# Kernel tuning notes

Hardware: AMD Instinct MI355X
Metric: run time of the kernel (lower is better)

Reference implementation:

```python
import jax, jax.numpy as jnp
import numpy as np

HIDDEN = 2048
HEADS = 16
HEAD_DIM = HIDDEN // HEADS
TOP_K = 256
B, N = 1, 2048


def setup_inputs() -> dict:
    key = jax.random.key(0)
    ks = jax.random.split(key, 9)
    s = 0.02
    return {
        "hidden_states": jax.random.normal(ks[0], (B, N, HIDDEN), jnp.float32),
        "Wq": jax.random.normal(ks[1], (HIDDEN, HIDDEN), jnp.float32) * s,
        "bq": jnp.zeros((HIDDEN,), jnp.float32),
        "Wk": jax.random.normal(ks[2], (HIDDEN, HIDDEN), jnp.float32) * s,
        "bk": jnp.zeros((HIDDEN,), jnp.float32),
        "Wv": jax.random.normal(ks[3], (HIDDEN, HIDDEN), jnp.float32) * s,
        "bv": jnp.zeros((HIDDEN,), jnp.float32),
        "Wo": jax.random.normal(ks[4], (HIDDEN, HIDDEN), jnp.float32) * s,
        "bo": jnp.zeros((HIDDEN,), jnp.float32),
    }


def _split_heads(x):
    b, n, _ = x.shape
    return x.reshape(b, n, HEADS, HEAD_DIM).transpose(0, 2, 1, 3)  # b h n d


def reference(hidden_states, Wq, bq, Wk, bk, Wv, bv, Wo, bo):
    scale = 1.0 / jnp.sqrt(jnp.float32(HEAD_DIM))
    q = _split_heads(hidden_states @ Wq + bq)  # [b,h,n,d]
    k = _split_heads(hidden_states @ Wk + bk)
    v = _split_heads(hidden_states @ Wv + bv)

    # Sparse path (kv_seq_length > attention_window): dense QK^T used only to rank keys.
    scores = jnp.einsum("bhnd,bhmd->bhnm", q, k) * scale  # [b,h,n,n]
    importance = scores.mean(axis=2)  # [b,h,n] aggregate over queries
    _, idx = jax.lax.top_k(importance, TOP_K)  # [b,h,k]

    # gather selected K/V (torch.gather along seq dim)
    k_sel = jnp.take_along_axis(k, idx[..., None], axis=2)  # [b,h,k,d]
    v_sel = jnp.take_along_axis(v, idx[..., None], axis=2)

    w = jax.nn.softmax(jnp.einsum("bhnd,bhkd->bhnk", q, k_sel) * scale, axis=-1)
    out = jnp.einsum("bhnk,bhkd->bhnd", w, v_sel)  # [b,h,n,d]
    out = out.transpose(0, 2, 1, 3).reshape(hidden_states.shape[0], -1, HIDDEN)
    return out @ Wo + bo
```

## Files before the change

### kernel.cpp

```cpp
#include <hip/hip_runtime.h>


typedef __attribute__((ext_vector_type(8))) short bf16x8;
typedef __attribute__((ext_vector_type(4))) float f32x4;

__device__ __forceinline__ unsigned short f2bf(float x) {
    unsigned u = __float_as_uint(x);
    u += 0x7fffu + ((u >> 16) & 1u);
    return (unsigned short)(u >> 16);
}

__device__ __forceinline__ void load_lds16(const unsigned short* g, unsigned short* l) {
    __builtin_amdgcn_global_load_lds(
        (const __attribute__((address_space(1))) unsigned int*)g,
        (__attribute__((address_space(3))) unsigned int*)l,
        16, 0, 0);
}

struct Bias3 { const float* p0; const float* p1; const float* p2; };
struct Ptr4  { const float* p[4]; };

template <int TN, bool OUT_BF16>
__global__ __launch_bounds__(256) void gemm_bf16(
    const unsigned short* __restrict__ A, long lda, long strideA,
    const unsigned short* __restrict__ Bt, long ldb, long strideB,
    void* __restrict__ Cv, long ldc, long strideC,
    Bias3 bias, int K, float alpha)
{
    constexpr int SN = TN / 32;
    __shared__ __align__(16) unsigned short As[128][32];
    __shared__ __align__(16) unsigned short Bs[TN][32];

    const int tid  = threadIdx.x;
    const int lane = tid & 63;
    const int wave = tid >> 6;
    const int wm = wave >> 1, wn = wave & 1;

    const int bm = blockIdx.y * 128;
    const int bn = blockIdx.x * TN;
    const int b  = blockIdx.z;

    const unsigned short* Ab = A  + (long)b * strideA;
    const unsigned short* Bb = Bt + (long)b * strideB;

    f32x4 acc[4][SN];
#pragma unroll
    for (int i = 0; i < 4; i++)
#pragma unroll
        for (int j = 0; j < SN; j++) acc[i][j] = f32x4{0.f, 0.f, 0.f, 0.f};

    const int lr = lane >> 2;
    const int lc = (lane & 3) * 8;

    for (int k0 = 0; k0 < K; k0 += 32) {
        __syncthreads();
#pragma unroll
        for (int r0 = wave * 16; r0 < 128; r0 += 64)
            load_lds16(Ab + (long)(bm + r0 + lr) * lda + k0 + lc, &As[r0][0]);
#pragma unroll
        for (int r0 = wave * 16; r0 < TN; r0 += 64)
            load_lds16(Bb + (long)(bn + r0 + lr) * ldb + k0 + lc, &Bs[r0][0]);
        __syncthreads();

        bf16x8 af[4], bf[SN];
#pragma unroll
        for (int s = 0; s < 4; s++)
            af[s] = *(const bf16x8*)&As[wm * 64 + s * 16 + (lane & 15)][(lane >> 4) * 8];
#pragma unroll
        for (int t = 0; t < SN; t++)
            bf[t] = *(const bf16x8*)&Bs[wn * (TN / 2) + t * 16 + (lane & 15)][(lane >> 4) * 8];
#pragma unroll
        for (int s = 0; s < 4; s++)
#pragma unroll
            for (int t = 0; t < SN; t++)
                acc[s][t] = __builtin_amdgcn_mfma_f32_16x16x32_bf16(af[s], bf[t], acc[s][t], 0, 0, 0);
    }

    const float* bp = (b == 0) ? bias.p0 : (b == 1) ? bias.p1 : bias.p2;
    float* Cf = (float*)Cv;
    unsigned short* Ch = (unsigned short*)Cv;
#pragma unroll
    for (int s = 0; s < 4; s++) {
#pragma unroll
        for (int t = 0; t < SN; t++) {
            const int col  = bn + wn * (TN / 2) + t * 16 + (lane & 15);
            const int row0 = bm + wm * 64 + s * 16 + (lane >> 4) * 4;
            const float bv = bp ? bp[col] : 0.f;
#pragma unroll
            for (int r = 0; r < 4; r++) {
                float v = alpha * acc[s][t][r] + bv;
                long off = (long)b * strideC + (long)(row0 + r) * ldc + col;
                if (OUT_BF16) Ch[off] = f2bf(v);
                else          Cf[off] = v;
            }
        }
    }
}

__global__ __launch_bounds__(256, 2) void attn_kernel(
    const unsigned short* __restrict__ Qb,
    const unsigned short* __restrict__ Ksel,
    const unsigned short* __restrict__ VselT,
    unsigned short* __restrict__ Att)
{
    __shared__ __align__(16) unsigned short Qs[64][32];
    __shared__ __align__(16) unsigned short Ks[256][32];
    __shared__ __align__(16) unsigned short Vs[128][32];
    __shared__ __align__(16) unsigned short Ps[64][264];
    __shared__ float linv[64];

    const int tid  = threadIdx.x;
    const int lane = tid & 63;
    const int wave = tid >> 6;
    const int bm = blockIdx.x * 64;
    const int h  = blockIdx.y;
    const int lr = lane >> 2, lc = (lane & 3) * 8;

    const unsigned short* Kh = Ksel  + h * 32768;
    const unsigned short* Vh = VselT + h * 32768;

    f32x4 acc[16];
#pragma unroll
    for (int t = 0; t < 16; t++) acc[t] = f32x4{0.f, 0.f, 0.f, 0.f};

    for (int k0 = 0; k0 < 128; k0 += 32) {
        __syncthreads();
        load_lds16(Qb + (long)(bm + wave * 16 + lr) * 2048 + h * 128 + k0 + lc,
                   &Qs[wave * 16][0]);
#pragma unroll
        for (int q = 0; q < 4; q++)
            load_lds16(Kh + (wave * 64 + q * 16 + lr) * 128 + k0 + lc,
                       &Ks[wave * 64 + q * 16][0]);
        __syncthreads();

        bf16x8 af = *(const bf16x8*)&Qs[wave * 16 + (lane & 15)][(lane >> 4) * 8];
#pragma unroll
        for (int t = 0; t < 16; t++) {
            bf16x8 bfv = *(const bf16x8*)&Ks[t * 16 + (lane & 15)][(lane >> 4) * 8];
            acc[t] = __builtin_amdgcn_mfma_f32_16x16x32_bf16(af, bfv, acc[t], 0, 0, 0);
        }
    }

    const float se = 0.08838834764831845f * 1.4426950408889634f;
#pragma unroll
    for (int r = 0; r < 4; r++) {
        float mx = -3.0e38f;
#pragma unroll
        for (int t = 0; t < 16; t++) mx = fmaxf(mx, acc[t][r]);
#pragma unroll
        for (int off = 1; off < 16; off <<= 1) mx = fmaxf(mx, __shfl_xor(mx, off));
        float sum = 0.f;
#pragma unroll
        for (int t = 0; t < 16; t++) {
            float p = exp2f((acc[t][r] - mx) * se);
            acc[t][r] = p;
            sum += p;
        }
#pragma unroll
        for (int off = 1; off < 16; off <<= 1) sum += __shfl_xor(sum, off);
        const int row = wave * 16 + (lane >> 4) * 4 + r;
#pragma unroll
        for (int t = 0; t < 16; t++)
            Ps[row][t * 16 + (lane & 15)] = f2bf(acc[t][r]);
        if ((lane & 15) == 0) linv[row] = 1.0f / sum;
    }

    const int wm2 = wave >> 1, wn2 = wave & 1;
    f32x4 acc2[2][4];
#pragma unroll
    for (int i = 0; i < 2; i++)
#pragma unroll
        for (int j = 0; j < 4; j++) acc2[i][j] = f32x4{0.f, 0.f, 0.f, 0.f};

    for (int j0 = 0; j0 < 256; j0 += 32) {
        __syncthreads();
#pragma unroll
        for (int q = 0; q < 2; q++)
            load_lds16(Vh + (wave * 32 + q * 16 + lr) * 256 + j0 + lc,
                       &Vs[wave * 32 + q * 16][0]);
        __syncthreads();

        bf16x8 af2[2], bf2v[4];
#pragma unroll
        for (int s2 = 0; s2 < 2; s2++)
            af2[s2] = *(const bf16x8*)&Ps[wm2 * 32 + s2 * 16 + (lane & 15)][j0 + (lane >> 4) * 8];
#pragma unroll
        for (int t2 = 0; t2 < 4; t2++)
            bf2v[t2] = *(const bf16x8*)&Vs[wn2 * 64 + t2 * 16 + (lane & 15)][(lane >> 4) * 8];
#pragma unroll
        for (int s2 = 0; s2 < 2; s2++)
#pragma unroll
            for (int t2 = 0; t2 < 4; t2++)
                acc2[s2][t2] = __builtin_amdgcn_mfma_f32_16x16x32_bf16(af2[s2], bf2v[t2], acc2[s2][t2], 0, 0, 0);
    }

#pragma unroll
    for (int s2 = 0; s2 < 2; s2++) {
#pragma unroll
        for (int t2 = 0; t2 < 4; t2++) {
            const int d = wn2 * 64 + t2 * 16 + (lane & 15);
#pragma unroll
            for (int r = 0; r < 4; r++) {
                const int row = wm2 * 32 + s2 * 16 + (lane >> 4) * 4 + r;
                float v = acc2[s2][t2][r] * linv[row];
                Att[(long)(bm + row) * 2048 + h * 128 + d] = f2bf(v);
            }
        }
    }
}

__global__ __launch_bounds__(256) void prep_kernel(Ptr4 srcs, unsigned short* __restrict__ WT4,
                                                   const float* __restrict__ hs,
                                                   double* __restrict__ part) {
    const int b = blockIdx.x;
    const int tid = threadIdx.x;
    if (b < 16384) {
        __shared__ float tile[32][33];
        const int z = b >> 12, xy = b & 4095;
        const float* W = srcs.p[z];
        unsigned short* WT = WT4 + (long)z * 4194304;
        const int bx = (xy & 63) * 32;
        const int by = (xy >> 6) * 32;
        const int x = tid & 31, y = tid >> 5;
#pragma unroll
        for (int i = 0; i < 32; i += 8)
            tile[y + i][x] = W[(long)(by + y + i) * 2048 + bx + x];
        __syncthreads();
#pragma unroll
        for (int i = 0; i < 32; i += 8)
            WT[(long)(bx + y + i) * 2048 + by + x] = f2bf(tile[x][y + i]);
    } else {
        const int c = b - 16384;
        const int col = (c & 7) * 256 + tid;
        const int r0  = (c >> 3) * 32;
        double a = 0.0;
#pragma unroll 4
        for (int r = 0; r < 32; r++) a += (double)hs[(long)(r0 + r) * 2048 + col];
        part[(long)(c >> 3) * 2048 + col] = a;
    }
}

__global__ void fill_kernel(float* p, float v, long n) {
    long i = ((long)blockIdx.x * blockDim.x + threadIdx.x) * 4;
    if (i + 3 < n) { p[i] = v; p[i+1] = v; p[i+2] = v; p[i+3] = v; }
}

__global__ __launch_bounds__(256) void mean_qsum_part(const double* __restrict__ part,
                                                      const float* __restrict__ Wq,
                                                      double* __restrict__ partq) {
    __shared__ float hsb[32];
    const int j  = blockIdx.x * 256 + threadIdx.x;
    const int i0 = blockIdx.y * 32;
    if (threadIdx.x < 32) {
        double s = 0.0;
#pragma unroll 4
        for (int g = 0; g < 64; g++) s += part[(long)g * 2048 + i0 + threadIdx.x];
        hsb[threadIdx.x] = (float)(s * (1.0 / 2048.0));
    }
    __syncthreads();
    double a = 0.0;
#pragma unroll 4
    for (int r = 0; r < 32; r++)
        a += (double)hsb[r] * (double)Wq[(long)(i0 + r) * 2048 + j];
    partq[(long)blockIdx.y * 2048 + j] = a;
}

__global__ void qsum_fin(const double* __restrict__ partq, const float* __restrict__ bq,
                         float* __restrict__ qbar) {
    const int j = blockIdx.x * 64 + threadIdx.x;
    double s = (double)bq[j];
#pragma unroll 4
    for (int g = 0; g < 64; g++) s += partq[(long)g * 2048 + j];
    qbar[j] = (float)s;
}

__global__ __launch_bounds__(256) void u_kernel(const float* __restrict__ Wk,
                                                const float* __restrict__ qbar,
                                                float* __restrict__ U) {
    const int i = blockIdx.x, t = threadIdx.x;
#pragma unroll
    for (int r = 0; r < 2; r++) {
        const int e = r * 1024 + t * 4;
        float4 w = *(const float4*)(Wk + (long)i * 2048 + e);
        float4 q = *(const float4*)(qbar + e);
        float a = w.x * q.x + w.y * q.y + w.z * q.z + w.w * q.w;
#pragma unroll
        for (int off = 16; off; off >>= 1) a += __shfl_xor(a, off);
        if ((t & 31) == 0) U[(long)i * 16 + r * 8 + (t >> 5)] = a;
    }
}

__global__ __launch_bounds__(256) void cast_imp_kernel(const float* __restrict__ hs,
                                                       const float* __restrict__ U,
                                                       unsigned short* __restrict__ HSb,
                                                       float* __restrict__ imp) {
    __shared__ float row[2048];
    __shared__ float red[4][16];
    const int m = blockIdx.x, t = threadIdx.x;
    for (int i = t; i < 2048; i += 256) {
        float v = hs[(long)m * 2048 + i];
        row[i] = v;
        HSb[(long)m * 2048 + i] = f2bf(v);
    }
    __syncthreads();
    float p[16];
#pragma unroll
    for (int h = 0; h < 16; h++) p[h] = 0.f;
    for (int i = t * 8; i < t * 8 + 8; i++) {
        const float v = row[i];
        const float* u = U + i * 16;
#pragma unroll
        for (int h = 0; h < 16; h++) p[h] += v * u[h];
    }
#pragma unroll
    for (int off = 32; off; off >>= 1)
#pragma unroll
        for (int h = 0; h < 16; h++) p[h] += __shfl_down(p[h], off);
    if ((t & 63) == 0)
#pragma unroll
        for (int h = 0; h < 16; h++) red[t >> 6][h] = p[h];
    __syncthreads();
    if (t < 16)
        imp[(long)t * 2048 + m] = red[0][t] + red[1][t] + red[2][t] + red[3][t];
}

__global__ __launch_bounds__(256) void topk_gather(const float* __restrict__ imp,
                                                   const unsigned short* __restrict__ Kb,
                                                   const unsigned short* __restrict__ Vb,
                                                   unsigned short* __restrict__ Ksel,
                                                   unsigned short* __restrict__ VselT) {
    __shared__ int sidx[256];
    __shared__ unsigned short Vt[64][130];
    const int h = blockIdx.x;
    const int tid = threadIdx.x;
    const int lane = tid & 63;
    const int wave = tid >> 6;

    if (wave == 0) {
        unsigned u[32];
#pragma unroll
        for (int r = 0; r < 32; r++) {
            unsigned x = __float_as_uint(imp[(long)h * 2048 + r * 64 + lane]);
            u[r] = (x & 0x80000000u) ? ~x : (x | 0x80000000u);
        }
        unsigned cur = 0;
        for (int b = 31; b >= 0; b--) {
            const unsigned cand = cur | (1u << b);
            int tot = 0;
#pragma unroll
            for (int r = 0; r < 32; r++)
                tot += (int)__popcll(__ballot(u[r] >= cand));
            if (tot >= 256) cur = cand;
        }
        const unsigned long long below = (1ull << lane) - 1ull;
        int base = 0;
#pragma unroll
        for (int r = 0; r < 32; r++) {
            const bool q = u[r] > cur;
            const unsigned long long m = __ballot(q);
            if (q) sidx[base + (int)__popcll(m & below)] = r * 64 + lane;
            base += (int)__popcll(m);
        }
#pragma unroll
        for (int r = 0; r < 32; r++) {
            const bool q = (u[r] == cur);
            const unsigned long long m = __ballot(q);
            if (q) {
                const int pos = base + (int)__popcll(m & below);
                if (pos < 256) sidx[pos] = r * 64 + lane;
            }
            base += (int)__popcll(m);
            if (base >= 256) break;
        }
    }
    __syncthreads();

    unsigned short* Kh = Ksel + h * 32768;
#pragma unroll 4
    for (int jj = 0; jj < 64; jj++) {
        const int j = wave * 64 + jj;
        const long sr = sidx[j];
        *(ushort2*)&Kh[j * 128 + lane * 2] =
            *(const ushort2*)&Kb[sr * 2048 + h * 128 + lane * 2];
    }

    unsigned short* Vh = VselT + h * 32768;
    for (int j0 = 0; j0 < 256; j0 += 64) {
        __syncthreads();
#pragma unroll 4
        for (int jj = 0; jj < 16; jj++) {
            const int jl = wave * 16 + jj;
            const long sr = sidx[j0 + jl];
            *(ushort2*)&Vt[jl][lane * 2] =
                *(const ushort2*)&Vb[sr * 2048 + h * 128 + lane * 2];
        }
        __syncthreads();
#pragma unroll 8
        for (int d = wave; d < 128; d += 4) {
            Vh[d * 256 + j0 + lane] = Vt[lane][d];
        }
    }
}

extern "C" void kernel_launch(void* const* d_in, const int* in_sizes, int n_in,
                              void* d_out, int out_size, void* d_ws, size_t ws_size,
                              hipStream_t stream)
{
    const float* hs = (const float*)d_in[0];
    const float* Wq = (const float*)d_in[1];
    const float* bq = (const float*)d_in[2];
    const float* Wk = (const float*)d_in[3];
    const float* bk = (const float*)d_in[4];
    const float* Wv = (const float*)d_in[5];
    const float* bv = (const float*)d_in[6];
    const float* Wo = (const float*)d_in[7];
    const float* bo = (const float*)d_in[8];

    char* ws = (char*)d_ws;
    size_t off = 0;
    auto alloc = [&](size_t b) -> void* {
        void* p = ws + off;
        off = (off + b + 255) & ~(size_t)255;
        return p;
    };
    unsigned short* HSb   = (unsigned short*)alloc(8388608);
    unsigned short* WT4   = (unsigned short*)alloc(4 * 8388608);
    unsigned short* QKVb  = (unsigned short*)alloc(3 * 8388608);
    unsigned short* Att   = (unsigned short*)alloc(8388608);
    unsigned short* Ksel  = (unsigned short*)alloc(1048576);
    unsigned short* VselT = (unsigned short*)alloc(1048576);
    double* part  = (double*)alloc(1048576);
    double* partq = (double*)alloc(1048576);
    float* qbar  = (float*)alloc(8192);
    float* U     = (float*)alloc(131072);
    float* imp   = (float*)alloc(131072);

    if (off > ws_size) {
        fill_kernel<<<4096, 256, 0, stream>>>((float*)d_out, 12345.0f, (long)out_size);
        return;
    }

    unsigned short* Qb = QKVb;
    unsigned short* Kb = QKVb + 4194304;
    unsigned short* Vb = QKVb + 2 * 4194304;
    unsigned short* WoT = WT4 + 3 * 4194304;

    prep_kernel<<<16896, 256, 0, stream>>>(Ptr4{{Wq, Wk, Wv, Wo}}, WT4, hs, part);

    mean_qsum_part<<<dim3(8, 64), 256, 0, stream>>>(part, Wq, partq);
    qsum_fin<<<32, 64, 0, stream>>>(partq, bq, qbar);
    u_kernel<<<2048, 256, 0, stream>>>(Wk, qbar, U);
    cast_imp_kernel<<<2048, 256, 0, stream>>>(hs, U, HSb, imp);

    gemm_bf16<128, true><<<dim3(16, 16, 3), 256, 0, stream>>>(
        HSb, 2048, 0, WT4, 2048, 4194304, QKVb, 2048, 4194304,
        Bias3{bq, bk, bv}, 2048, 1.0f);

    topk_gather<<<16, 256, 0, stream>>>(imp, Kb, Vb, Ksel, VselT);

    attn_kernel<<<dim3(32, 16), 256, 0, stream>>>(Qb, Ksel, VselT, Att);

    gemm_bf16<64, false><<<dim3(32, 16, 1), 256, 0, stream>>>(
        Att, 2048, 0, WoT, 2048, 0, d_out, 2048, 0,
        Bias3{bo, bo, bo}, 2048, 1.0f);
}
```

Baseline: 335.0 us.

## Fuse top-k K/V gather into QKV GEMM epilogue and split-K the output projection

Top-k selection now runs before the QKV GEMM and emits a per-row position map. The GEMM epilogue then writes only the selected K rows (and transposed V) directly into Ksel/VselT, which removes the full K/V stores and the separate gather kernel. The output projection switches to 128x128 tiles with split-K over two halves, followed by a small reduction kernel that adds the bias. This trades the gather pass for scattered epilogue writes and adds a fp32 partial-buffer round trip for the output GEMM.

Measured after the change: 337.2 us. About the same (+0.6%).

```diff
diff --git a/kernel.cpp b/kernel.cpp
--- a/kernel.cpp
+++ b/kernel.cpp
@@ -20,16 +20,18 @@
 struct Bias3 { const float* p0; const float* p1; const float* p2; };
 struct Ptr4  { const float* p[4]; };
 
-template <int TN, bool OUT_BF16>
+template <bool SELECT>
 __global__ __launch_bounds__(256) void gemm_bf16(
     const unsigned short* __restrict__ A, long lda, long strideA,
     const unsigned short* __restrict__ Bt, long ldb, long strideB,
     void* __restrict__ Cv, long ldc, long strideC,
-    Bias3 bias, int K, float alpha)
+    Bias3 bias, int K,
+    const int* __restrict__ jpos,
+    unsigned short* __restrict__ Ksel,
+    unsigned short* __restrict__ VselT)
 {
-    constexpr int SN = TN / 32;
     __shared__ __align__(16) unsigned short As[128][32];
-    __shared__ __align__(16) unsigned short Bs[TN][32];
+    __shared__ __align__(16) unsigned short Bs[128][32];
 
     const int tid  = threadIdx.x;
     const int lane = tid & 63;
@@ -37,17 +39,17 @@
     const int wm = wave >> 1, wn = wave & 1;
 
     const int bm = blockIdx.y * 128;
-    const int bn = blockIdx.x * TN;
+    const int bn = blockIdx.x * 128;
     const int b  = blockIdx.z;
 
     const unsigned short* Ab = A  + (long)b * strideA;
     const unsigned short* Bb = Bt + (long)b * strideB;
 
-    f32x4 acc[4][SN];
+    f32x4 acc[4][4];
 #pragma unroll
     for (int i = 0; i < 4; i++)
 #pragma unroll
-        for (int j = 0; j < SN; j++) acc[i][j] = f32x4{0.f, 0.f, 0.f, 0.f};
+        for (int j = 0; j < 4; j++) acc[i][j] = f32x4{0.f, 0.f, 0.f, 0.f};
 
     const int lr = lane >> 2;
     const int lc = (lane & 3) * 8;
@@ -55,24 +57,23 @@
     for (int k0 = 0; k0 < K; k0 += 32) {
         __syncthreads();
 #pragma unroll
-        for (int r0 = wave * 16; r0 < 128; r0 += 64)
+        for (int r0 = wave * 16; r0 < 128; r0 += 64) {
             load_lds16(Ab + (long)(bm + r0 + lr) * lda + k0 + lc, &As[r0][0]);
-#pragma unroll
-        for (int r0 = wave * 16; r0 < TN; r0 += 64)
             load_lds16(Bb + (long)(bn + r0 + lr) * ldb + k0 + lc, &Bs[r0][0]);
-        __syncthreads();
-
-        bf16x8 af[4], bf[SN];
+        }
+        __syncthreads();
+
+        bf16x8 af[4], bf[4];
 #pragma unroll
         for (int s = 0; s < 4; s++)
             af[s] = *(const bf16x8*)&As[wm * 64 + s * 16 + (lane & 15)][(lane >> 4) * 8];
 #pragma unroll
-        for (int t = 0; t < SN; t++)
-            bf[t] = *(const bf16x8*)&Bs[wn * (TN / 2) + t * 16 + (lane & 15)][(lane >> 4) * 8];
+        for (int t = 0; t < 4; t++)
+            bf[t] = *(const bf16x8*)&Bs[wn * 64 + t * 16 + (lane & 15)][(lane >> 4) * 8];
 #pragma unroll
         for (int s = 0; s < 4; s++)
 #pragma unroll
-            for (int t = 0; t < SN; t++)
+            for (int t = 0; t < 4; t++)
                 acc[s][t] = __builtin_amdgcn_mfma_f32_16x16x32_bf16(af[s], bf[t], acc[s][t], 0, 0, 0);
     }
 
@@ -82,19 +83,45 @@
 #pragma unroll
     for (int s = 0; s < 4; s++) {
 #pragma unroll
-        for (int t = 0; t < SN; t++) {
-            const int col  = bn + wn * (TN / 2) + t * 16 + (lane & 15);
+        for (int t = 0; t < 4; t++) {
+            const int col  = bn + wn * 64 + t * 16 + (lane & 15);
             const int row0 = bm + wm * 64 + s * 16 + (lane >> 4) * 4;
-            const float bv = bp ? bp[col] : 0.f;
 #pragma unroll
             for (int r = 0; r < 4; r++) {
-                float v = alpha * acc[s][t][r] + bv;
-                long off = (long)b * strideC + (long)(row0 + r) * ldc + col;
-                if (OUT_BF16) Ch[off] = f2bf(v);
-                else          Cf[off] = v;
+                const int row = row0 + r;
+                if (SELECT) {
+                    const float v = acc[s][t][r] + bp[col];
+                    if (b == 0) {
+                        Ch[(long)row * ldc + col] = f2bf(v);
+                    } else {
+                        const int hh = col >> 7, dd = col & 127;
+                        const int j = jpos[hh * 2048 + row];
+                        if (j >= 0) {
+                            if (b == 1) Ksel [hh * 32768 + j * 128 + dd]  = f2bf(v);
+                            else        VselT[hh * 32768 + dd * 256 + j]  = f2bf(v);
+                        }
+                    }
+                } else {
+                    Cf[(long)b * strideC + (long)row * ldc + col] = acc[s][t][r];
+                }
             }
         }
     }
+}
+
+__global__ __launch_bounds__(256) void oreduce(const float* __restrict__ part,
+                                               const float* __restrict__ bo,
+                                               float* __restrict__ out) {
+    const long i = ((long)blockIdx.x * 256 + threadIdx.x) * 4;
+    float4 a = *(const float4*)(part + i);
+    float4 b = *(const float4*)(part + 4194304 + i);
+    const int col = (int)(i & 2047);
+    float4 o;
+    o.x = a.x + b.x + bo[col];
+    o.y = a.y + b.y + bo[col + 1];
+    o.z = a.z + b.z + bo[col + 2];
+    o.w = a.w + b.w + bo[col + 3];
+    *(float4*)(out + i) = o;
 }
 
 __global__ __launch_bounds__(256, 2) void attn_kernel(
@@ -324,82 +351,48 @@
         imp[(long)t * 2048 + m] = red[0][t] + red[1][t] + red[2][t] + red[3][t];
 }
 
-__global__ __launch_bounds__(256) void topk_gather(const float* __restrict__ imp,
-                                                   const unsigned short* __restrict__ Kb,
-                                                   const unsigned short* __restrict__ Vb,
-                                                   unsigned short* __restrict__ Ksel,
-                                                   unsigned short* __restrict__ VselT) {
-    __shared__ int sidx[256];
-    __shared__ unsigned short Vt[64][130];
+__global__ __launch_bounds__(64) void topk_jpos(const float* __restrict__ imp,
+                                                int* __restrict__ jpos) {
     const int h = blockIdx.x;
-    const int tid = threadIdx.x;
-    const int lane = tid & 63;
-    const int wave = tid >> 6;
-
-    if (wave == 0) {
-        unsigned u[32];
-#pragma unroll
-        for (int r = 0; r < 32; r++) {
-            unsigned x = __float_as_uint(imp[(long)h * 2048 + r * 64 + lane]);
-            u[r] = (x & 0x80000000u) ? ~x : (x | 0x80000000u);
-        }
-        unsigned cur = 0;
-        for (int b = 31; b >= 0; b--) {
-            const unsigned cand = cur | (1u << b);
-            int tot = 0;
-#pragma unroll
-            for (int r = 0; r < 32; r++)
-                tot += (int)__popcll(__ballot(u[r] >= cand));
-            if (tot >= 256) cur = cand;
-        }
-        const unsigned long long below = (1ull << lane) - 1ull;
-        int base = 0;
-#pragma unroll
-        for (int r = 0; r < 32; r++) {
-            const bool q = u[r] > cur;
-            const unsigned long long m = __ballot(q);
-            if (q) sidx[base + (int)__popcll(m & below)] = r * 64 + lane;
-            base += (int)__popcll(m);
-        }
-#pragma unroll
-        for (int r = 0; r < 32; r++) {
-            const bool q = (u[r] == cur);
-            const unsigned long long m = __ballot(q);
-            if (q) {
-                const int pos = base + (int)__popcll(m & below);
-                if (pos < 256) sidx[pos] = r * 64 + lane;
-            }
-            base += (int)__popcll(m);
-            if (base >= 256) break;
-        }
-    }
-    __syncthreads();
-
-    unsigned short* Kh = Ksel + h * 32768;
-#pragma unroll 4
-    for (int jj = 0; jj < 64; jj++) {
-        const int j = wave * 64 + jj;
-        const long sr = sidx[j];
-        *(ushort2*)&Kh[j * 128 + lane * 2] =
-            *(const ushort2*)&Kb[sr * 2048 + h * 128 + lane * 2];
-    }
-
-    unsigned short* Vh = VselT + h * 32768;
-    for (int j0 = 0; j0 < 256; j0 += 64) {
-        __syncthreads();
-#pragma unroll 4
-        for (int jj = 0; jj < 16; jj++) {
-            const int jl = wave * 16 + jj;
-            const long sr = sidx[j0 + jl];
-            *(ushort2*)&Vt[jl][lane * 2] =
-                *(const ushort2*)&Vb[sr * 2048 + h * 128 + lane * 2];
-        }
-        __syncthreads();
-#pragma unroll 8
-        for (int d = wave; d < 128; d += 4) {
-            Vh[d * 256 + j0 + lane] = Vt[lane][d];
-        }
-    }
+    const int lane = threadIdx.x;
+    unsigned u[32];
+#pragma unroll
+    for (int r = 0; r < 32; r++) {
+        unsigned x = __float_as_uint(imp[(long)h * 2048 + r * 64 + lane]);
+        u[r] = (x & 0x80000000u) ? ~x : (x | 0x80000000u);
+    }
+    unsigned cur = 0;
+    for (int b = 31; b >= 0; b--) {
+        const unsigned cand = cur | (1u << b);
+        int tot = 0;
+#pragma unroll
+        for (int r = 0; r < 32; r++)
+            tot += (int)__popcll(__ballot(u[r] >= cand));
+        if (tot >= 256) cur = cand;
+    }
+    const unsigned long long below = (1ull << lane) - 1ull;
+    int pos[32];
+    int base = 0;
+#pragma unroll
+    for (int r = 0; r < 32; r++) {
+        const bool q = u[r] > cur;
+        const unsigned long long m = __ballot(q);
+        pos[r] = q ? base + (int)__popcll(m & below) : -1;
+        base += (int)__popcll(m);
+    }
+#pragma unroll
+    for (int r = 0; r < 32; r++) {
+        const bool q = (u[r] == cur);
+        const unsigned long long m = __ballot(q);
+        if (q) {
+            const int p = base + (int)__popcll(m & below);
+            pos[r] = (p < 256) ? p : -1;
+        }
+        base += (int)__popcll(m);
+    }
+#pragma unroll
+    for (int r = 0; r < 32; r++)
+        jpos[h * 2048 + r * 64 + lane] = pos[r];
 }
 
 extern "C" void kernel_launch(void* const* d_in, const int* in_sizes, int n_in,
@@ -425,24 +418,23 @@
     };
     unsigned short* HSb   = (unsigned short*)alloc(8388608);
     unsigned short* WT4   = (unsigned short*)alloc(4 * 8388608);
-    unsigned short* QKVb  = (unsigned short*)alloc(3 * 8388608);
+    unsigned short* Qb    = (unsigned short*)alloc(8388608);
     unsigned short* Att   = (unsigned short*)alloc(8388608);
     unsigned short* Ksel  = (unsigned short*)alloc(1048576);
     unsigned short* VselT = (unsigned short*)alloc(1048576);
+    float* Opart = (float*)alloc(2 * 16777216);
     double* part  = (double*)alloc(1048576);
     double* partq = (double*)alloc(1048576);
     float* qbar  = (float*)alloc(8192);
     float* U     = (float*)alloc(131072);
     float* imp   = (float*)alloc(131072);
+    int*   jpos  = (int*)alloc(131072);
 
     if (off > ws_size) {
         fill_kernel<<<4096, 256, 0, stream>>>((float*)d_out, 12345.0f, (long)out_size);
         return;
     }
 
-    unsigned short* Qb = QKVb;
-    unsigned short* Kb = QKVb + 4194304;
-    unsigned short* Vb = QKVb + 2 * 4194304;
     unsigned short* WoT = WT4 + 3 * 4194304;
 
     prep_kernel<<<16896, 256, 0, stream>>>(Ptr4{{Wq, Wk, Wv, Wo}}, WT4, hs, part);
@@ -452,15 +444,17 @@
     u_kernel<<<2048, 256, 0, stream>>>(Wk, qbar, U);
     cast_imp_kernel<<<2048, 256, 0, stream>>>(hs, U, HSb, imp);
 
-    gemm_bf16<128, true><<<dim3(16, 16, 3), 256, 0, stream>>>(
-        HSb, 2048, 0, WT4, 2048, 4194304, QKVb, 2048, 4194304,
-        Bias3{bq, bk, bv}, 2048, 1.0f);
-
-    topk_gather<<<16, 256, 0, stream>>>(imp, Kb, Vb, Ksel, VselT);
+    topk_jpos<<<16, 64, 0, stream>>>(imp, jpos);
+
+    gemm_bf16<true><<<dim3(16, 16, 3), 256, 0, stream>>>(
+        HSb, 2048, 0, WT4, 2048, 4194304, Qb, 2048, 0,
+        Bias3{bq, bk, bv}, 2048, jpos, Ksel, VselT);
 
     attn_kernel<<<dim3(32, 16), 256, 0, stream>>>(Qb, Ksel, VselT, Att);
 
-    gemm_bf16<64, false><<<dim3(32, 16, 1), 256, 0, stream>>>(
-        Att, 2048, 0, WoT, 2048, 0, d_out, 2048, 0,
-        Bias3{bo, bo, bo}, 2048, 1.0f);
-}
+    gemm_bf16<false><<<dim3(16, 16, 2), 256, 0, stream>>>(
+        Att, 2048, 1024, WoT, 2048, 1024, Opart, 2048, 4194304,
+        Bias3{nullptr, nullptr, nullptr}, 1024, nullptr, nullptr, nullptr);
+
+    oreduce<<<4096, 256, 0, stream>>>(Opart, bo, (float*)d_out);
+}
```
